# Kernel tuning notes

Hardware: AMD Instinct MI355X
Metric: run time of the kernel (lower is better)

Reference implementation:

```python
import jax, jax.numpy as jnp
import numpy as np

B, T, D, H = 64, 2048, 256, 512

def setup_inputs() -> dict:
    key = jax.random.key(0)
    kx, kw, ku, kb = jax.random.split(key, 4)
    s_in = 1.0 / np.sqrt(H)
    x = jax.random.normal(kx, (B, T, D), dtype=jnp.float32)
    W = jax.random.uniform(kw, (D, 4 * H), dtype=jnp.float32, minval=-s_in, maxval=s_in)
    U = jax.random.uniform(ku, (H, 4 * H), dtype=jnp.float32, minval=-s_in, maxval=s_in)
    b = jax.random.uniform(kb, (4 * H,), dtype=jnp.float32, minval=-s_in, maxval=s_in)
    return {"x": x, "W": W, "U": U, "b": b}

def _lstm_scan(x, W, U, b):
    # Precompute input projections for all timesteps: [B, T, 4H]
    xW = jnp.einsum('btd,dg->btg', x, W) + b
    h0 = jnp.zeros((x.shape[0], H), dtype=x.dtype)
    c0 = jnp.zeros((x.shape[0], H), dtype=x.dtype)

    def step(carry, xw_t):
        h, c = carry
        gates = xw_t + h @ U  # [B, 4H]
        i, f, g, o = jnp.split(gates, 4, axis=-1)
        i = jax.nn.sigmoid(i)
        f = jax.nn.sigmoid(f)
        g = jnp.tanh(g)
        o = jax.nn.sigmoid(o)
        c_new = f * c + i * g
        h_new = o * jnp.tanh(c_new)
        return (h_new, c_new), None

    (h_t, c_t), _ = jax.lax.scan(step, (h0, c0), jnp.swapaxes(xW, 0, 1))
    return h_t, c_t

def reference(x, W, U, b):
    # Returns final (h_t, c_t), matching LSTM_encoder.forward
    return _lstm_scan(x, W, U, b)
```

## Files before the change

kernel.cpp:

```cpp
#include <hip/hip_runtime.h>
#include <hip/hip_bf16.h>


#define B_   64
#define T_   2048
#define D_   256
#define H_   512
#define G4   2048
#define KK   24
#define TILES 4
#define UWP  40
#define BSTR (64 * UWP)

#define OFF_UWL 0
#define SZ_UWL  (KK * 64 * UWP * 2)
#define OFF_ZH  (OFF_UWL + SZ_UWL)
#define SZ_ZH   (16 * 512 * 2)
#define OFF_ZX  (OFF_ZH + SZ_ZH)
#define SZ_ZX   (2 * 16 * 256 * 2)
#define OFF_GT  (OFF_ZX + SZ_ZX)
#define SZ_GT   (4 * 16 * 17 * 4)
#define OFF_BS  (OFF_GT + SZ_GT)
#define SZ_BS   (64 * 4)
#define SMEM_BYTES (OFF_BS + SZ_BS)

typedef __attribute__((ext_vector_type(8))) short v8s;
typedef __attribute__((ext_vector_type(4))) float v4f;
typedef unsigned long long u64;

__device__ __forceinline__ unsigned short f2bf(float f) {
    unsigned u = __builtin_bit_cast(unsigned, f);
    u = (u + 0x7FFFu + ((u >> 16) & 1u)) >> 16;
    return (unsigned short)u;
}
__device__ __forceinline__ u64 pack4(float4 v) {
    return (u64)((unsigned)f2bf(v.x) | ((unsigned)f2bf(v.y) << 16)) |
           ((u64)((unsigned)f2bf(v.z) | ((unsigned)f2bf(v.w) << 16)) << 32);
}
__device__ __forceinline__ float fast_sigmoid(float v) {
    return 1.0f / (1.0f + __expf(-v));
}
__device__ __forceinline__ float fast_tanh(float v) {
    float x = fminf(fmaxf(v, -15.0f), 15.0f);
    float e = __expf(2.0f * x);
    return (e - 1.0f) / (e + 1.0f);
}

__global__ void __launch_bounds__(256, 1)
lstm_persist(const float* __restrict__ x, const float* __restrict__ W,
             const float* __restrict__ U, const float* __restrict__ bias,
             float* __restrict__ out, u64* __restrict__ hbuf )
{
    extern __shared__ char smem[];
    unsigned short* UWL = (unsigned short*)(smem + OFF_UWL);
    char*           zhB = smem + OFF_ZH;
    char*           zxB = smem + OFF_ZX;
    float*          gt  = (float*)(smem + OFF_GT);
    float*          bs  = (float*)(smem + OFF_BS);

    const int tid  = threadIdx.x;
    const int g    = blockIdx.x;
    const int tile = g & (TILES - 1);
    const int s    = g >> 2;
    const int l    = tid & 63;
    const int w    = tid >> 6;
    const int pb   = tid >> 4;
    const int jj   = tid & 15;

    for (int idx = tid; idx < (H_ + D_) * 64; idx += 256) {
        int k = idx >> 6;
        int n = idx & 63;
        int gcol = (n >> 4) * H_ + s * 16 + (n & 15);
        float v = (k < H_) ? U[(size_t)k * G4 + gcol]
                           : W[(size_t)(k - H_) * G4 + gcol];
        UWL[((k >> 5) * 64 + n) * UWP + (k & 31)] = f2bf(v);
    }
    if (tid < 64) {
        int gcol = (tid >> 4) * H_ + s * 16 + (tid & 15);
        bs[tid] = bias[gcol];
    }
    for (int n = tid; n < 2048; n += 256)
        *(u64*)(zhB + n * 8) = 0ull;
    #pragma unroll
    for (int p = 0; p < 4; ++p) {
        int n = p * 256 + tid;
        int row = n >> 6, c4 = n & 63;
        float4 v = *(const float4*)(x + ((size_t)(tile * 16 + row) * T_ + 0) * D_ + c4 * 4);
        *(u64*)(zxB + row * 512 + ((c4 * 8) ^ ((row & 7) << 4))) = pack4(v);
    }

    const int r    = l & 15;
    const int q    = l >> 4;
    const int krot = (r >> 2) & 1;
    const int qx   = (q ^ (r & 3)) << 4;
    const int ahoff0 = r * 1024 + qx + 64 * krot;
    const int ahoff1 = r * 1024 + qx + 64 * (krot ^ 1);
    const int axoff0 = r * 512  + qx + 64 * krot;
    const int axoff1 = r * 512  + qx + 64 * (krot ^ 1);
    const unsigned short* brow = UWL + (w * 16 + r) * UWP + q * 8;

    float creg = 0.0f;
    __syncthreads();

    for (int t = 0; t < T_; ++t) {
        u64 hv[16];
        u64* hb = hbuf + (size_t)((t - 1) & 1) * 16384 + (size_t)tile * 4096;
        if (t > 0) {
            #pragma unroll
            for (int p = 0; p < 16; ++p)
                hv[p] = __hip_atomic_load(hb + p * 256 + tid,
                                          __ATOMIC_RELAXED, __HIP_MEMORY_SCOPE_AGENT);
        }
        float4 xr[4];
        if (t < T_ - 1) {
            #pragma unroll
            for (int p = 0; p < 4; ++p) {
                int n = p * 256 + tid, row = n >> 6, c4 = n & 63;
                xr[p] = *(const float4*)
                    (x + ((size_t)(tile * 16 + row) * T_ + (t + 1)) * D_ + c4 * 4);
            }
        }

        const char* axb = zxB + (t & 1) * 8192;
        v4f xc0 = {0,0,0,0}, xc1 = {0,0,0,0}, xc2 = {0,0,0,0}, xc3 = {0,0,0,0};
        {
            v8s a0 = *(const v8s*)(axb + axoff0 + 0);
            v8s b0 = *(const v8s*)(brow + (size_t)16 * BSTR);
            xc0 = __builtin_amdgcn_mfma_f32_16x16x32_bf16(a0, b0, xc0, 0, 0, 0);
            v8s a1 = *(const v8s*)(axb + axoff1 + 0);
            v8s b1 = *(const v8s*)(brow + (size_t)17 * BSTR);
            xc1 = __builtin_amdgcn_mfma_f32_16x16x32_bf16(a1, b1, xc1, 0, 0, 0);
            v8s a2 = *(const v8s*)(axb + axoff0 + 128);
            v8s b2 = *(const v8s*)(brow + (size_t)18 * BSTR);
            xc2 = __builtin_amdgcn_mfma_f32_16x16x32_bf16(a2, b2, xc2, 0, 0, 0);
            v8s a3 = *(const v8s*)(axb + axoff1 + 128);
            v8s b3 = *(const v8s*)(brow + (size_t)19 * BSTR);
            xc3 = __builtin_amdgcn_mfma_f32_16x16x32_bf16(a3, b3, xc3, 0, 0, 0);
            v8s a4 = *(const v8s*)(axb + axoff0 + 256);
            v8s b4 = *(const v8s*)(brow + (size_t)20 * BSTR);
            xc0 = __builtin_amdgcn_mfma_f32_16x16x32_bf16(a4, b4, xc0, 0, 0, 0);
            v8s a5 = *(const v8s*)(axb + axoff1 + 256);
            v8s b5 = *(const v8s*)(brow + (size_t)21 * BSTR);
            xc1 = __builtin_amdgcn_mfma_f32_16x16x32_bf16(a5, b5, xc1, 0, 0, 0);
            v8s a6 = *(const v8s*)(axb + axoff0 + 384);
            v8s b6 = *(const v8s*)(brow + (size_t)22 * BSTR);
            xc2 = __builtin_amdgcn_mfma_f32_16x16x32_bf16(a6, b6, xc2, 0, 0, 0);
            v8s a7 = *(const v8s*)(axb + axoff1 + 384);
            v8s b7 = *(const v8s*)(brow + (size_t)23 * BSTR);
            xc3 = __builtin_amdgcn_mfma_f32_16x16x32_bf16(a7, b7, xc3, 0, 0, 0);
        }

        if (t > 0) {
            const unsigned tg = (unsigned)(t - 1);
            unsigned pend = 0u;
            #pragma unroll
            for (int p = 0; p < 16; ++p)
                pend |= ((unsigned)hv[p] != tg) ? (1u << p) : 0u;
            while (pend) {
                #pragma unroll
                for (int p = 0; p < 16; ++p)
                    if (pend & (1u << p))
                        hv[p] = __hip_atomic_load(hb + p * 256 + tid,
                                    __ATOMIC_RELAXED, __HIP_MEMORY_SCOPE_AGENT);
                unsigned np = 0u;
                #pragma unroll
                for (int p = 0; p < 16; ++p)
                    np |= ((unsigned)hv[p] != tg) ? (1u << p) : 0u;
                pend = np;
            }
            #pragma unroll
            for (int p = 0; p < 16; ++p) {
                int swz = (p & 7) << 4;
                *(unsigned*)(zhB + p * 1024 + ((tid * 4) ^ swz)) =
                    (unsigned)(hv[p] >> 32);
            }
        }
        __syncthreads();

        v4f ac0 = {0,0,0,0}, ac1 = {0,0,0,0}, ac2 = {0,0,0,0}, ac3 = {0,0,0,0};
        #pragma unroll
        for (int kk = 0; kk < 16; kk += 4) {
            v8s a0 = *(const v8s*)(zhB + ahoff0 + 128 * (kk >> 1));
            v8s b0 = *(const v8s*)(brow + (size_t)(kk + 0) * BSTR);
            ac0 = __builtin_amdgcn_mfma_f32_16x16x32_bf16(a0, b0, ac0, 0, 0, 0);
            v8s a1 = *(const v8s*)(zhB + ahoff1 + 128 * (kk >> 1));
            v8s b1 = *(const v8s*)(brow + (size_t)(kk + 1) * BSTR);
            ac1 = __builtin_amdgcn_mfma_f32_16x16x32_bf16(a1, b1, ac1, 0, 0, 0);
            v8s a2 = *(const v8s*)(zhB + ahoff0 + 128 * (kk >> 1) + 128);
            v8s b2 = *(const v8s*)(brow + (size_t)(kk + 2) * BSTR);
            ac2 = __builtin_amdgcn_mfma_f32_16x16x32_bf16(a2, b2, ac2, 0, 0, 0);
            v8s a3 = *(const v8s*)(zhB + ahoff1 + 128 * (kk >> 1) + 128);
            v8s b3 = *(const v8s*)(brow + (size_t)(kk + 3) * BSTR);
            ac3 = __builtin_amdgcn_mfma_f32_16x16x32_bf16(a3, b3, ac3, 0, 0, 0);
        }

        if (t < T_ - 1) {
            char* zxn = zxB + ((t + 1) & 1) * 8192;
            #pragma unroll
            for (int p = 0; p < 4; ++p) {
                int n = p * 256 + tid, row = n >> 6, c4 = n & 63;
                *(u64*)(zxn + row * 512 + ((c4 * 8) ^ ((row & 7) << 4))) = pack4(xr[p]);
            }
        }

        {
            v4f acc = ((ac0 + ac1) + (ac2 + ac3)) + ((xc0 + xc1) + (xc2 + xc3));
            float bcol = bs[w * 16 + r];
            #pragma unroll
            for (int rr = 0; rr < 4; ++rr) {
                float v = acc[rr] + bcol;
                float a = (w == 2) ? fast_tanh(v) : fast_sigmoid(v);
                gt[(w * 16 + (q * 4 + rr)) * 17 + r] = a;
            }
        }
        __syncthreads();

        float iv = gt[(0 * 16 + pb) * 17 + jj];
        float fv = gt[(1 * 16 + pb) * 17 + jj];
        float gv = gt[(2 * 16 + pb) * 17 + jj];
        float ov = gt[(3 * 16 + pb) * 17 + jj];
        float cn = fv * creg + iv * gv;
        creg = cn;
        float h = ov * fast_tanh(cn);

        if (t == T_ - 1) {
            out[(size_t)(tile * 16 + pb) * H_ + s * 16 + jj] = h;
            out[(size_t)B_ * H_ + (size_t)(tile * 16 + pb) * H_ + s * 16 + jj] = cn;
        } else {
            unsigned hu = (unsigned)f2bf(h);
            unsigned nb = (unsigned)__shfl_xor((int)hu, 1, 64);
            if ((jj & 1) == 0) {
                u64 pv = ((u64)(hu | (nb << 16)) << 32) | (u64)(unsigned)t;
                __hip_atomic_store(hbuf + (size_t)(t & 1) * 16384
                                        + (size_t)(tile * 16 + pb) * 256
                                        + s * 8 + (jj >> 1),
                                   pv, __ATOMIC_RELAXED, __HIP_MEMORY_SCOPE_AGENT);
            }
        }
    }
}

extern "C" void kernel_launch(void* const* d_in, const int* in_sizes, int n_in,
                              void* d_out, int out_size, void* d_ws, size_t ws_size,
                              hipStream_t stream) {
    const float* x  = (const float*)d_in[0];
    const float* W  = (const float*)d_in[1];
    const float* U  = (const float*)d_in[2];
    const float* bb = (const float*)d_in[3];
    float* out = (float*)d_out;

    u64* hbuf = (u64*)d_ws;

    hipMemsetAsync(d_ws, 0xFF, (size_t)2 * 64 * 256 * 8, stream);

    hipFuncSetAttribute((const void*)lstm_persist,
                        hipFuncAttributeMaxDynamicSharedMemorySize, SMEM_BYTES);

    lstm_persist<<<TILES * 32, 256, SMEM_BYTES, stream>>>(
        x, W, U, bb, out, hbuf);
}
```

Measured before the change: 8.010 ms.

## Fuse gate activations in registers via shuffles, double-buffer h and drop a barrier

Reorders the B-operand column mapping so each wave holds the i/f/g/o gates for the same hidden units. The cell update is then done in registers through lane shuffles, which removes the gt shared-memory round trip and one __syncthreads per timestep. The h staging buffer is double-buffered, and each block writes its own h slice straight into shared memory, skipping the poll for its own columns. Next-step h polling loads and x prefetch are issued earlier to hide latency. It also uses the hardware packed bf16 convert, a unified sigmoid/tanh formula, and a smaller LDS pad, with added risk in the ordering of the shared-memory double buffer.

```diff
diff --git a/kernel.cpp b/kernel.cpp
--- a/kernel.cpp
+++ b/kernel.cpp
@@ -7,22 +7,17 @@
 #define D_   256
 #define H_   512
 #define G4   2048
-#define KK   24
 #define TILES 4
-#define UWP  40
+#define UWP  34
 #define BSTR (64 * UWP)
 
 #define OFF_UWL 0
-#define SZ_UWL  (KK * 64 * UWP * 2)
+#define SZ_UWL  (24 * 64 * UWP * 2)
 #define OFF_ZH  (OFF_UWL + SZ_UWL)
-#define SZ_ZH   (16 * 512 * 2)
+#define SZ_ZH   (2 * 16 * 512 * 2)
 #define OFF_ZX  (OFF_ZH + SZ_ZH)
 #define SZ_ZX   (2 * 16 * 256 * 2)
-#define OFF_GT  (OFF_ZX + SZ_ZX)
-#define SZ_GT   (4 * 16 * 17 * 4)
-#define OFF_BS  (OFF_GT + SZ_GT)
-#define SZ_BS   (64 * 4)
-#define SMEM_BYTES (OFF_BS + SZ_BS)
+#define SMEM_BYTES (OFF_ZX + SZ_ZX)
 
 typedef __attribute__((ext_vector_type(8))) short v8s;
 typedef __attribute__((ext_vector_type(4))) float v4f;
@@ -33,12 +28,15 @@
     u = (u + 0x7FFFu + ((u >> 16) & 1u)) >> 16;
     return (unsigned short)u;
 }
+__device__ __forceinline__ unsigned cvt_pk_bf16(float lo, float hi) {
+    unsigned r;
+    asm volatile("v_cvt_pk_bf16_f32 %0, %1, %2" : "=v"(r) : "v"(lo), "v"(hi));
+    return r;
+}
 __device__ __forceinline__ u64 pack4(float4 v) {
-    return (u64)((unsigned)f2bf(v.x) | ((unsigned)f2bf(v.y) << 16)) |
-           ((u64)((unsigned)f2bf(v.z) | ((unsigned)f2bf(v.w) << 16)) << 32);
-}
-__device__ __forceinline__ float fast_sigmoid(float v) {
-    return 1.0f / (1.0f + __expf(-v));
+    unsigned lo = cvt_pk_bf16(v.x, v.y);
+    unsigned hi = cvt_pk_bf16(v.z, v.w);
+    return (u64)lo | ((u64)hi << 32);
 }
 __device__ __forceinline__ float fast_tanh(float v) {
     float x = fminf(fmaxf(v, -15.0f), 15.0f);
@@ -55,8 +53,6 @@
     unsigned short* UWL = (unsigned short*)(smem + OFF_UWL);
     char*           zhB = smem + OFF_ZH;
     char*           zxB = smem + OFF_ZX;
-    float*          gt  = (float*)(smem + OFF_GT);
-    float*          bs  = (float*)(smem + OFF_BS);
 
     const int tid  = threadIdx.x;
     const int g    = blockIdx.x;
@@ -64,8 +60,13 @@
     const int s    = g >> 2;
     const int l    = tid & 63;
     const int w    = tid >> 6;
-    const int pb   = tid >> 4;
-    const int jj   = tid & 15;
+    const int bn   = l & 15;
+    const int gi   = bn >> 2;
+    const int cc   = bn & 3;
+    const int q4   = l >> 4;
+    const bool isG = (gi == 2);
+    const bool gi0 = (gi == 0);
+    const bool own = ((tid >> 3) == s);
 
     for (int idx = tid; idx < (H_ + D_) * 64; idx += 256) {
         int k = idx >> 6;
@@ -75,10 +76,11 @@
                            : W[(size_t)(k - H_) * G4 + gcol];
         UWL[((k >> 5) * 64 + n) * UWP + (k & 31)] = f2bf(v);
     }
-    if (tid < 64) {
-        int gcol = (tid >> 4) * H_ + s * 16 + (tid & 15);
-        bs[tid] = bias[gcol];
-    }
+    const float breg = bias[gi * H_ + s * 16 + w * 4 + cc];
+    const float oM = isG ? 2.0f : 1.0f;
+    const float oA = isG ? -1.0f : 0.0f;
+    const float aM = isG ? 2.0f : 1.0f;
+
     for (int n = tid; n < 2048; n += 256)
         *(u64*)(zhB + n * 8) = 0ull;
     #pragma unroll
@@ -88,39 +90,28 @@
         float4 v = *(const float4*)(x + ((size_t)(tile * 16 + row) * T_ + 0) * D_ + c4 * 4);
         *(u64*)(zxB + row * 512 + ((c4 * 8) ^ ((row & 7) << 4))) = pack4(v);
     }
-
-    const int r    = l & 15;
-    const int q    = l >> 4;
+    float4 xr[4];
+    #pragma unroll
+    for (int p = 0; p < 4; ++p) {
+        int n = p * 256 + tid, row = n >> 6, c4 = n & 63;
+        xr[p] = *(const float4*)(x + ((size_t)(tile * 16 + row) * T_ + 1) * D_ + c4 * 4);
+    }
+
+    const int r    = bn;
     const int krot = (r >> 2) & 1;
-    const int qx   = (q ^ (r & 3)) << 4;
+    const int qx   = (q4 ^ (r & 3)) << 4;
     const int ahoff0 = r * 1024 + qx + 64 * krot;
     const int ahoff1 = r * 1024 + qx + 64 * (krot ^ 1);
     const int axoff0 = r * 512  + qx + 64 * krot;
     const int axoff1 = r * 512  + qx + 64 * (krot ^ 1);
-    const unsigned short* brow = UWL + (w * 16 + r) * UWP + q * 8;
-
-    float creg = 0.0f;
+    const unsigned short* brow = UWL + (gi * 16 + w * 4 + cc) * UWP + q4 * 8;
+    const int col2o = s * 8 + w * 2 + (cc >> 1);
+
+    u64 hv[16];
+    float creg[4] = {0.0f, 0.0f, 0.0f, 0.0f};
     __syncthreads();
 
     for (int t = 0; t < T_; ++t) {
-        u64 hv[16];
-        u64* hb = hbuf + (size_t)((t - 1) & 1) * 16384 + (size_t)tile * 4096;
-        if (t > 0) {
-            #pragma unroll
-            for (int p = 0; p < 16; ++p)
-                hv[p] = __hip_atomic_load(hb + p * 256 + tid,
-                                          __ATOMIC_RELAXED, __HIP_MEMORY_SCOPE_AGENT);
-        }
-        float4 xr[4];
-        if (t < T_ - 1) {
-            #pragma unroll
-            for (int p = 0; p < 4; ++p) {
-                int n = p * 256 + tid, row = n >> 6, c4 = n & 63;
-                xr[p] = *(const float4*)
-                    (x + ((size_t)(tile * 16 + row) * T_ + (t + 1)) * D_ + c4 * 4);
-            }
-        }
-
         const char* axb = zxB + (t & 1) * 8192;
         v4f xc0 = {0,0,0,0}, xc1 = {0,0,0,0}, xc2 = {0,0,0,0}, xc3 = {0,0,0,0};
         {
@@ -152,46 +143,32 @@
 
         if (t > 0) {
             const unsigned tg = (unsigned)(t - 1);
-            unsigned pend = 0u;
-            #pragma unroll
-            for (int p = 0; p < 16; ++p)
-                pend |= ((unsigned)hv[p] != tg) ? (1u << p) : 0u;
-            while (pend) {
+            const u64* hbp = hbuf + (size_t)((t - 1) & 1) * 16384
+                                  + (size_t)tile * 4096;
+            if (!own) {
+                unsigned pend = 0u;
                 #pragma unroll
                 for (int p = 0; p < 16; ++p)
-                    if (pend & (1u << p))
-                        hv[p] = __hip_atomic_load(hb + p * 256 + tid,
-                                    __ATOMIC_RELAXED, __HIP_MEMORY_SCOPE_AGENT);
-                unsigned np = 0u;
-                #pragma unroll
-                for (int p = 0; p < 16; ++p)
-                    np |= ((unsigned)hv[p] != tg) ? (1u << p) : 0u;
-                pend = np;
-            }
-            #pragma unroll
-            for (int p = 0; p < 16; ++p) {
-                int swz = (p & 7) << 4;
-                *(unsigned*)(zhB + p * 1024 + ((tid * 4) ^ swz)) =
-                    (unsigned)(hv[p] >> 32);
-            }
-        }
-        __syncthreads();
-
-        v4f ac0 = {0,0,0,0}, ac1 = {0,0,0,0}, ac2 = {0,0,0,0}, ac3 = {0,0,0,0};
-        #pragma unroll
-        for (int kk = 0; kk < 16; kk += 4) {
-            v8s a0 = *(const v8s*)(zhB + ahoff0 + 128 * (kk >> 1));
-            v8s b0 = *(const v8s*)(brow + (size_t)(kk + 0) * BSTR);
-            ac0 = __builtin_amdgcn_mfma_f32_16x16x32_bf16(a0, b0, ac0, 0, 0, 0);
-            v8s a1 = *(const v8s*)(zhB + ahoff1 + 128 * (kk >> 1));
-            v8s b1 = *(const v8s*)(brow + (size_t)(kk + 1) * BSTR);
-            ac1 = __builtin_amdgcn_mfma_f32_16x16x32_bf16(a1, b1, ac1, 0, 0, 0);
-            v8s a2 = *(const v8s*)(zhB + ahoff0 + 128 * (kk >> 1) + 128);
-            v8s b2 = *(const v8s*)(brow + (size_t)(kk + 2) * BSTR);
-            ac2 = __builtin_amdgcn_mfma_f32_16x16x32_bf16(a2, b2, ac2, 0, 0, 0);
-            v8s a3 = *(const v8s*)(zhB + ahoff1 + 128 * (kk >> 1) + 128);
-            v8s b3 = *(const v8s*)(brow + (size_t)(kk + 3) * BSTR);
-            ac3 = __builtin_amdgcn_mfma_f32_16x16x32_bf16(a3, b3, ac3, 0, 0, 0);
+                    pend |= ((unsigned)((unsigned)hv[p] != tg)) << p;
+                while (pend) {
+                    #pragma unroll
+                    for (int p = 0; p < 16; ++p)
+                        if (pend & (1u << p))
+                            hv[p] = __hip_atomic_load(hbp + p * 256 + tid,
+                                        __ATOMIC_RELAXED, __HIP_MEMORY_SCOPE_AGENT);
+                    unsigned np = 0u;
+                    #pragma unroll
+                    for (int p = 0; p < 16; ++p)
+                        np |= ((unsigned)((unsigned)hv[p] != tg)) << p;
+                    pend = np;
+                }
+                char* zht = zhB + (t & 1) * 16384;
+                #pragma unroll
+                for (int p = 0; p < 16; ++p) {
+                    *(unsigned*)(zht + p * 1024 + ((tid * 4) ^ ((p & 7) << 4))) =
+                        (unsigned)(hv[p] >> 32);
+                }
+            }
         }
 
         if (t < T_ - 1) {
@@ -201,40 +178,91 @@
                 int n = p * 256 + tid, row = n >> 6, c4 = n & 63;
                 *(u64*)(zxn + row * 512 + ((c4 * 8) ^ ((row & 7) << 4))) = pack4(xr[p]);
             }
-        }
-
-        {
-            v4f acc = ((ac0 + ac1) + (ac2 + ac3)) + ((xc0 + xc1) + (xc2 + xc3));
-            float bcol = bs[w * 16 + r];
+            int tt = (t + 2 < T_) ? t + 2 : T_ - 1;
             #pragma unroll
-            for (int rr = 0; rr < 4; ++rr) {
-                float v = acc[rr] + bcol;
-                float a = (w == 2) ? fast_tanh(v) : fast_sigmoid(v);
-                gt[(w * 16 + (q * 4 + rr)) * 17 + r] = a;
+            for (int p = 0; p < 4; ++p) {
+                int n = p * 256 + tid, row = n >> 6, c4 = n & 63;
+                xr[p] = *(const float4*)
+                    (x + ((size_t)(tile * 16 + row) * T_ + tt) * D_ + c4 * 4);
             }
         }
         __syncthreads();
 
-        float iv = gt[(0 * 16 + pb) * 17 + jj];
-        float fv = gt[(1 * 16 + pb) * 17 + jj];
-        float gv = gt[(2 * 16 + pb) * 17 + jj];
-        float ov = gt[(3 * 16 + pb) * 17 + jj];
-        float cn = fv * creg + iv * gv;
-        creg = cn;
-        float h = ov * fast_tanh(cn);
+        const char* zht = zhB + (t & 1) * 16384;
+        v4f ac0 = {0,0,0,0}, ac1 = {0,0,0,0}, ac2 = {0,0,0,0}, ac3 = {0,0,0,0};
+        #pragma unroll
+        for (int kk = 0; kk < 16; kk += 4) {
+            v8s a0 = *(const v8s*)(zht + ahoff0 + 128 * (kk >> 1));
+            v8s b0 = *(const v8s*)(brow + (size_t)(kk + 0) * BSTR);
+            ac0 = __builtin_amdgcn_mfma_f32_16x16x32_bf16(a0, b0, ac0, 0, 0, 0);
+            v8s a1 = *(const v8s*)(zht + ahoff1 + 128 * (kk >> 1));
+            v8s b1 = *(const v8s*)(brow + (size_t)(kk + 1) * BSTR);
+            ac1 = __builtin_amdgcn_mfma_f32_16x16x32_bf16(a1, b1, ac1, 0, 0, 0);
+            v8s a2 = *(const v8s*)(zht + ahoff0 + 128 * (kk >> 1) + 128);
+            v8s b2 = *(const v8s*)(brow + (size_t)(kk + 2) * BSTR);
+            ac2 = __builtin_amdgcn_mfma_f32_16x16x32_bf16(a2, b2, ac2, 0, 0, 0);
+            v8s a3 = *(const v8s*)(zht + ahoff1 + 128 * (kk >> 1) + 128);
+            v8s b3 = *(const v8s*)(brow + (size_t)(kk + 3) * BSTR);
+            ac3 = __builtin_amdgcn_mfma_f32_16x16x32_bf16(a3, b3, ac3, 0, 0, 0);
+        }
+
+        v4f acc = ((ac0 + ac1) + (ac2 + ac3)) + ((xc0 + xc1) + (xc2 + xc3));
+        float hval[4], cnl[4];
+        #pragma unroll
+        for (int rr = 0; rr < 4; ++rr) {
+            float v = acc[rr] + breg;
+            float e = __expf(-aM * v);
+            float sg = 1.0f / (1.0f + e);
+            float a  = sg * oM + oA;
+            float fA = __shfl_xor(a, 4, 64);
+            float gA = __shfl_xor(a, 8, 64);
+            float oAv = __shfl_xor(a, 12, 64);
+            float cn = fA * creg[rr] + a * gA;
+            creg[rr] = cn;
+            cnl[rr] = cn;
+            hval[rr] = oAv * fast_tanh(cn);
+        }
 
         if (t == T_ - 1) {
-            out[(size_t)(tile * 16 + pb) * H_ + s * 16 + jj] = h;
-            out[(size_t)B_ * H_ + (size_t)(tile * 16 + pb) * H_ + s * 16 + jj] = cn;
+            if (gi0) {
+                #pragma unroll
+                for (int rr = 0; rr < 4; ++rr) {
+                    int grow = tile * 16 + q4 * 4 + rr;
+                    int col  = s * 16 + w * 4 + cc;
+                    out[(size_t)grow * H_ + col] = hval[rr];
+                    out[(size_t)B_ * H_ + (size_t)grow * H_ + col] = cnl[rr];
+                }
+            }
         } else {
-            unsigned hu = (unsigned)f2bf(h);
-            unsigned nb = (unsigned)__shfl_xor((int)hu, 1, 64);
-            if ((jj & 1) == 0) {
-                u64 pv = ((u64)(hu | (nb << 16)) << 32) | (u64)(unsigned)t;
-                __hip_atomic_store(hbuf + (size_t)(t & 1) * 16384
-                                        + (size_t)(tile * 16 + pb) * 256
-                                        + s * 8 + (jj >> 1),
-                                   pv, __ATOMIC_RELAXED, __HIP_MEMORY_SCOPE_AGENT);
+            const u64* hbn = hbuf + (size_t)(t & 1) * 16384 + (size_t)tile * 4096;
+            if (!own) {
+                #pragma unroll
+                for (int p = 0; p < 16; ++p)
+                    hv[p] = __hip_atomic_load(hbn + p * 256 + tid,
+                                __ATOMIC_RELAXED, __HIP_MEMORY_SCOPE_AGENT);
+            }
+            asm volatile("" ::: "memory");
+            unsigned hu0 = (unsigned)f2bf(hval[0]);
+            unsigned hu1 = (unsigned)f2bf(hval[1]);
+            unsigned hu2 = (unsigned)f2bf(hval[2]);
+            unsigned hu3 = (unsigned)f2bf(hval[3]);
+            unsigned p0 = hu0 | ((unsigned)__shfl_xor((int)hu0, 1, 64) << 16);
+            unsigned p1 = hu1 | ((unsigned)__shfl_xor((int)hu1, 1, 64) << 16);
+            unsigned p2 = hu2 | ((unsigned)__shfl_xor((int)hu2, 1, 64) << 16);
+            unsigned p3 = hu3 | ((unsigned)__shfl_xor((int)hu3, 1, 64) << 16);
+            if (gi0 && ((cc & 1) == 0)) {
+                u64* hbw = hbuf + (size_t)(t & 1) * 16384;
+                char* zhn = zhB + ((t + 1) & 1) * 16384;
+                unsigned pr[4] = {p0, p1, p2, p3};
+                #pragma unroll
+                for (int rr = 0; rr < 4; ++rr) {
+                    int row = q4 * 4 + rr;
+                    u64 pv = ((u64)pr[rr] << 32) | (u64)(unsigned)t;
+                    __hip_atomic_store(hbw + (size_t)(tile * 16 + row) * 256 + col2o,
+                                       pv, __ATOMIC_RELAXED, __HIP_MEMORY_SCOPE_AGENT);
+                    *(unsigned*)(zhn + row * 1024 +
+                                 ((col2o * 4) ^ ((row & 7) << 4))) = pr[rr];
+                }
             }
         }
     }
```

Result: slower. 19.29 ms (+140.9%).
